# Optimization experiments

Hardware: AMD Instinct MI355X
Metric: run time of the kernel (lower is better)

The kernel has to match this reference:

```python
import jax, jax.numpy as jnp
import numpy as np
import itertools

N_OBJECTS = 8
NUM_VARS = 2  # num_total_variables


def _perm_indices(num_objects: int, num_vars: int):
    """Static permutation indices, matching AndLayer.build()."""
    perm_idxs = np.array(list(itertools.permutations(range(num_objects), num_vars)))  # [K, V]
    binary_idxs = np.stack(np.nonzero(1 - np.eye(num_vars))).T  # [V*(V-1), 2]
    binary_idxs = binary_idxs.reshape(num_vars, num_vars - 1, 2)
    perm_bidxs = perm_idxs[:, binary_idxs]  # [K, V, V-1, 2]
    shift = (perm_bidxs[..., 1] > perm_bidxs[..., 0]).astype(np.int64)
    perm_bidxs = np.stack([perm_bidxs[..., 0], perm_bidxs[..., 1] - shift], axis=-1)
    return perm_idxs, perm_bidxs


def setup_inputs() -> dict:
    key = jax.random.key(0)
    k0, k1, k2, k3 = jax.random.split(key, 4)
    B, N, P0, P1, P2, C = 32, N_OBJECTS, 64, 128, 64, 128
    V = NUM_VARS
    num_in = P0 + V * P1 + V * (V - 1) * P2  # 448
    return {
        "nullary_preds": jax.random.uniform(k0, (B, P0), dtype=jnp.float32),
        "unary_preds": jax.random.uniform(k1, (B, N, P1), dtype=jnp.float32),
        "binary_preds": jax.random.uniform(k2, (B, N, N - 1, P2), dtype=jnp.float32),
        "kernel": jax.random.normal(k3, (num_in, C), dtype=jnp.float32),
    }


def reference(nullary_preds, unary_preds, binary_preds, kernel):
    B = nullary_preds.shape[0]
    N = unary_preds.shape[1]
    perm_idxs, perm_bidxs = _perm_indices(N, NUM_VARS)
    K = perm_idxs.shape[0]  # number of permutations

    # [B, K, P0]
    perm_nullary = jnp.broadcast_to(nullary_preds[:, None], (B, K) + nullary_preds.shape[1:])
    # gather over object axis: [B, K, V, P1]
    perm_unary = unary_preds[:, perm_idxs]
    # gather (i, j') pairs: [B, K, V, V-1, P2]
    perm_binary = binary_preds[:, perm_bidxs[..., 0], perm_bidxs[..., 1]]

    in_tensor = jnp.concatenate(
        [perm_nullary,
         perm_unary.reshape(B, K, -1),
         perm_binary.reshape(B, K, -1)], axis=-1)  # [B, K, num_in]

    k = jnp.tanh(kernel)  # [num_in, C]
    # [B, K, num_in, C]
    weighted_truth = in_tensor[..., None] * k + (1.0 - jnp.square(k))
    conjuncts = jnp.max(jnp.min(weighted_truth, axis=2), axis=1)  # [B, C]
    return conjuncts
```

## Files before the change

### kernel.cpp

```cpp
#include <hip/hip_runtime.h>
#include <math.h>

#define BATCH   32
#define NOBJ    8
#define P0      64
#define P1      128
#define P2      64
#define COUT    128
#define KPERM   56
#define ITOT    448
#define NBGB    4
#define NIH     8
#define ISEG    (ITOT / NIH)
#define IC      8
#define NBLK    (KPERM * NBGB)
#define POISON  0xAAAAAAAAu

#define AMAX_ELEMS 4096
#define CNT_OFF    4096

__device__ __forceinline__ unsigned enc3(float f) {
    return __float_as_uint(f + 3.0f) | 0x80000000u;
}
__device__ __forceinline__ float dec3(unsigned u) {
    return __uint_as_float(u & 0x7FFFFFFFu) - 3.0f;
}
__device__ __forceinline__ float4 min4(float4 a, float4 b) {
    return make_float4(fminf(a.x, b.x), fminf(a.y, b.y),
                       fminf(a.z, b.z), fminf(a.w, b.w));
}
__device__ __forceinline__ float fast_tanh(float x) {
    const float e = __expf(2.0f * x);
    return fmaf(-2.0f, __builtin_amdgcn_rcpf(e + 1.0f), 1.0f);
}

__global__ __launch_bounds__(1024) void and_fused(const float* __restrict__ nullary,
                                                  const float* __restrict__ unary,
                                                  const float* __restrict__ binary,
                                                  const float* __restrict__ kern,
                                                  unsigned* __restrict__ ws,
                                                  float* __restrict__ out) {
    __shared__ float4 xs[ITOT][2];
    __shared__ float4 pm[NIH][COUT][2];
    __shared__ unsigned lastflag;

    unsigned* __restrict__ amax    = ws;
    unsigned* __restrict__ counter = ws + CNT_OFF;

    const int blk = blockIdx.x;
    const int k   = blk >> 2;
    const int bg  = blk & 3;
    const int tid = threadIdx.x;
    const int c   = tid & (COUT - 1);
    const int ih  = tid >> 7;

    const int a = k / (NOBJ - 1);
    const int r = k % (NOBJ - 1);
    const int bobj = r + (r >= a ? 1 : 0);
    const int m0 = bobj - (bobj > a ? 1 : 0);
    const int m1 = a - (a > bobj ? 1 : 0);

    float* xsf = (float*)xs;
    for (int e = tid; e < ITOT * 8; e += 1024) {
        const int i  = e >> 3;
        const int lb = e & 7;
        const int b  = bg * 8 + lb;
        float v;
        if (i < P0) {
            v = nullary[b * P0 + i];
        } else if (i < P0 + 2 * P1) {
            const int t2 = i - P0;
            const int vv = t2 >> 7;
            const int p  = t2 & (P1 - 1);
            const int n  = vv ? bobj : a;
            v = unary[(b * NOBJ + n) * P1 + p];
        } else {
            const int t2 = i - (P0 + 2 * P1);
            const int vv = t2 >> 6;
            const int p  = t2 & (P2 - 1);
            const int n  = vv ? bobj : a;
            const int m  = vv ? m1 : m0;
            v = binary[((b * NOBJ + n) * (NOBJ - 1) + m) * P2 + p];
        }
        xsf[e] = v;
    }
    __syncthreads();

    const float* __restrict__ kp = kern + c;
    float4 accL = make_float4(INFINITY, INFINITY, INFINITY, INFINITY);
    float4 accH = accL;

    const int ibase = ih * ISEG;
    #pragma unroll
    for (int i0 = ibase; i0 < ibase + ISEG; i0 += IC) {
        float kv[IC];
        #pragma unroll
        for (int u = 0; u < IC; ++u) kv[u] = kp[(i0 + u) << 7];
        #pragma unroll
        for (int u = 0; u < IC; ++u) {
            const float t  = fast_tanh(kv[u]);
            const float bs = fmaf(-t, t, 1.0f);
            const float4 xl = xs[i0 + u][0];
            const float4 xh = xs[i0 + u][1];
            accL.x = fminf(accL.x, fmaf(xl.x, t, bs));
            accL.y = fminf(accL.y, fmaf(xl.y, t, bs));
            accL.z = fminf(accL.z, fmaf(xl.z, t, bs));
            accL.w = fminf(accL.w, fmaf(xl.w, t, bs));
            accH.x = fminf(accH.x, fmaf(xh.x, t, bs));
            accH.y = fminf(accH.y, fmaf(xh.y, t, bs));
            accH.z = fminf(accH.z, fmaf(xh.z, t, bs));
            accH.w = fminf(accH.w, fmaf(xh.w, t, bs));
        }
    }

    pm[ih][c][0] = accL;
    pm[ih][c][1] = accH;
    __syncthreads();

    if (ih == 0) {
        float4 lo = pm[0][c][0], hi = pm[0][c][1];
        #pragma unroll
        for (int q = 1; q < NIH; ++q) {
            lo = min4(lo, pm[q][c][0]);
            hi = min4(hi, pm[q][c][1]);
        }
        unsigned* base = amax + (bg * 8) * COUT + c;
        atomicMax(base + 0 * COUT, enc3(lo.x));
        atomicMax(base + 1 * COUT, enc3(lo.y));
        atomicMax(base + 2 * COUT, enc3(lo.z));
        atomicMax(base + 3 * COUT, enc3(lo.w));
        atomicMax(base + 4 * COUT, enc3(hi.x));
        atomicMax(base + 5 * COUT, enc3(hi.y));
        atomicMax(base + 6 * COUT, enc3(hi.z));
        atomicMax(base + 7 * COUT, enc3(hi.w));
    }

    __syncthreads();
    if (tid == 0) {
        __threadfence();
        lastflag = (atomicAdd(counter, 1u) == POISON + (unsigned)(NBLK - 1));
    }
    __syncthreads();
    if (lastflag) {
        __threadfence();
        #pragma unroll
        for (int e = tid; e < AMAX_ELEMS; e += 1024) {
            const unsigned u = atomicAdd(amax + e, 0u);
            out[e] = dec3(u);
        }
    }
}

extern "C" void kernel_launch(void* const* d_in, const int* in_sizes, int n_in,
                              void* d_out, int out_size, void* d_ws, size_t ws_size,
                              hipStream_t stream) {
    const float* nullary = (const float*)d_in[0];
    const float* unary   = (const float*)d_in[1];
    const float* binary  = (const float*)d_in[2];
    const float* kern    = (const float*)d_in[3];
    float* out = (float*)d_out;

    and_fused<<<NBLK, 1024, 0, stream>>>(nullary, unary, binary, kern,
                                         (unsigned*)d_ws, out);
}
```

Measured before the change: 77.03 us.

## Split into gather/tanh prep kernel and main min-max kernel reading global staging

Splits the fused kernel into two launches. The first computes tanh(kernel) once into workspace and writes the gathered per-block input tiles to global memory. The second reads the precomputed tanh values and the 8-wide input vectors straight from global memory (no LDS staging), using paired min3 reductions with a smaller unroll. This drops the tanh that every block recomputed for each element and the shared-memory staging barrier. In exchange it adds a kernel launch and a global round-trip of about 3.2 MB for the gathered inputs.

New measurement: 77.33 us. About the same (+0.4%).

```diff
diff --git a/kernel.cpp b/kernel.cpp
--- a/kernel.cpp
+++ b/kernel.cpp
@@ -12,12 +12,15 @@
 #define NBGB    4
 #define NIH     8
 #define ISEG    (ITOT / NIH)
-#define IC      8
+#define IC      4
 #define NBLK    (KPERM * NBGB)
+#define XPB     (ITOT * 8)
 #define POISON  0xAAAAAAAAu
 
 #define AMAX_ELEMS 4096
 #define CNT_OFF    4096
+#define X_OFF      8192
+#define TK_OFF     (X_OFF + NBLK * XPB)
 
 __device__ __forceinline__ unsigned enc3(float f) {
     return __float_as_uint(f + 3.0f) | 0x80000000u;
@@ -25,43 +28,38 @@
 __device__ __forceinline__ float dec3(unsigned u) {
     return __uint_as_float(u & 0x7FFFFFFFu) - 3.0f;
 }
+__device__ __forceinline__ float min3f(float a, float b, float c) {
+    return fminf(fminf(a, b), c);
+}
 __device__ __forceinline__ float4 min4(float4 a, float4 b) {
     return make_float4(fminf(a.x, b.x), fminf(a.y, b.y),
                        fminf(a.z, b.z), fminf(a.w, b.w));
 }
-__device__ __forceinline__ float fast_tanh(float x) {
-    const float e = __expf(2.0f * x);
-    return fmaf(-2.0f, __builtin_amdgcn_rcpf(e + 1.0f), 1.0f);
-}
 
-__global__ __launch_bounds__(1024) void and_fused(const float* __restrict__ nullary,
-                                                  const float* __restrict__ unary,
-                                                  const float* __restrict__ binary,
-                                                  const float* __restrict__ kern,
-                                                  unsigned* __restrict__ ws,
-                                                  float* __restrict__ out) {
-    __shared__ float4 xs[ITOT][2];
-    __shared__ float4 pm[NIH][COUT][2];
-    __shared__ unsigned lastflag;
+typedef __attribute__((ext_vector_type(8))) float f32x8;
 
-    unsigned* __restrict__ amax    = ws;
-    unsigned* __restrict__ counter = ws + CNT_OFF;
+__global__ __launch_bounds__(1024) void prep_gather(const float* __restrict__ nullary,
+                                                    const float* __restrict__ unary,
+                                                    const float* __restrict__ binary,
+                                                    const float* __restrict__ kern,
+                                                    float* __restrict__ tk,
+                                                    float* __restrict__ X) {
+    const int blk = blockIdx.x;
+    const int tid = threadIdx.x;
 
-    const int blk = blockIdx.x;
-    const int k   = blk >> 2;
-    const int bg  = blk & 3;
-    const int tid = threadIdx.x;
-    const int c   = tid & (COUT - 1);
-    const int ih  = tid >> 7;
+    const int tkidx = blk * 1024 + tid;
+    if (tkidx < ITOT * COUT) tk[tkidx] = tanhf(kern[tkidx]);
 
+    const int k  = blk >> 2;
+    const int bg = blk & 3;
     const int a = k / (NOBJ - 1);
     const int r = k % (NOBJ - 1);
     const int bobj = r + (r >= a ? 1 : 0);
     const int m0 = bobj - (bobj > a ? 1 : 0);
     const int m1 = a - (a > bobj ? 1 : 0);
 
-    float* xsf = (float*)xs;
-    for (int e = tid; e < ITOT * 8; e += 1024) {
+    float* __restrict__ Xb = X + blk * XPB;
+    for (int e = tid; e < XPB; e += 1024) {
         const int i  = e >> 3;
         const int lb = e & 7;
         const int b  = bg * 8 + lb;
@@ -82,34 +80,57 @@
             const int m  = vv ? m1 : m0;
             v = binary[((b * NOBJ + n) * (NOBJ - 1) + m) * P2 + p];
         }
-        xsf[e] = v;
+        Xb[e] = v;
     }
-    __syncthreads();
+}
 
-    const float* __restrict__ kp = kern + c;
+__global__ __launch_bounds__(1024) void and_main(const float* __restrict__ tk,
+                                                 const float* __restrict__ X,
+                                                 unsigned* __restrict__ ws,
+                                                 float* __restrict__ out) {
+    __shared__ float4 pm[NIH][COUT][2];
+    __shared__ unsigned lastflag;
+
+    unsigned* __restrict__ amax    = ws;
+    unsigned* __restrict__ counter = ws + CNT_OFF;
+
+    const int blk = blockIdx.x;
+    const int bg  = blk & 3;
+    const int tid = threadIdx.x;
+    const int c   = tid & (COUT - 1);
+    const int ih  = tid >> 7;
+
+    const unsigned xoff =
+        (unsigned)__builtin_amdgcn_readfirstlane(blk * XPB + ih * ISEG * 8);
+    const f32x8* __restrict__ Xv = (const f32x8*)(X + xoff);
+
+    const float* __restrict__ tkp = tk + c;
+    const int ibase = ih * ISEG;
+
     float4 accL = make_float4(INFINITY, INFINITY, INFINITY, INFINITY);
     float4 accH = accL;
 
-    const int ibase = ih * ISEG;
-    #pragma unroll
-    for (int i0 = ibase; i0 < ibase + ISEG; i0 += IC) {
-        float kv[IC];
+    for (int c0 = 0; c0 < ISEG; c0 += IC) {
+        float  tv[IC];
+        f32x8  xv[IC];
         #pragma unroll
-        for (int u = 0; u < IC; ++u) kv[u] = kp[(i0 + u) << 7];
+        for (int u = 0; u < IC; ++u) tv[u] = tkp[(ibase + c0 + u) << 7];
         #pragma unroll
-        for (int u = 0; u < IC; ++u) {
-            const float t  = fast_tanh(kv[u]);
-            const float bs = fmaf(-t, t, 1.0f);
-            const float4 xl = xs[i0 + u][0];
-            const float4 xh = xs[i0 + u][1];
-            accL.x = fminf(accL.x, fmaf(xl.x, t, bs));
-            accL.y = fminf(accL.y, fmaf(xl.y, t, bs));
-            accL.z = fminf(accL.z, fmaf(xl.z, t, bs));
-            accL.w = fminf(accL.w, fmaf(xl.w, t, bs));
-            accH.x = fminf(accH.x, fmaf(xh.x, t, bs));
-            accH.y = fminf(accH.y, fmaf(xh.y, t, bs));
-            accH.z = fminf(accH.z, fmaf(xh.z, t, bs));
-            accH.w = fminf(accH.w, fmaf(xh.w, t, bs));
+        for (int u = 0; u < IC; ++u) xv[u] = Xv[c0 + u];
+        #pragma unroll
+        for (int u = 0; u < IC; u += 2) {
+            const float ta  = tv[u],   tb  = tv[u + 1];
+            const float bsa = fmaf(-ta, ta, 1.0f);
+            const float bsb = fmaf(-tb, tb, 1.0f);
+            const f32x8 xa = xv[u], xb = xv[u + 1];
+            accL.x = min3f(accL.x, fmaf(xa[0], ta, bsa), fmaf(xb[0], tb, bsb));
+            accL.y = min3f(accL.y, fmaf(xa[1], ta, bsa), fmaf(xb[1], tb, bsb));
+            accL.z = min3f(accL.z, fmaf(xa[2], ta, bsa), fmaf(xb[2], tb, bsb));
+            accL.w = min3f(accL.w, fmaf(xa[3], ta, bsa), fmaf(xb[3], tb, bsb));
+            accH.x = min3f(accH.x, fmaf(xa[4], ta, bsa), fmaf(xb[4], tb, bsb));
+            accH.y = min3f(accH.y, fmaf(xa[5], ta, bsa), fmaf(xb[5], tb, bsb));
+            accH.z = min3f(accH.z, fmaf(xa[6], ta, bsa), fmaf(xb[6], tb, bsb));
+            accH.w = min3f(accH.w, fmaf(xa[7], ta, bsa), fmaf(xb[7], tb, bsb));
         }
     }
 
@@ -160,6 +181,10 @@
     const float* kern    = (const float*)d_in[3];
     float* out = (float*)d_out;
 
-    and_fused<<<NBLK, 1024, 0, stream>>>(nullary, unary, binary, kern,
-                                         (unsigned*)d_ws, out);
+    unsigned* ws = (unsigned*)d_ws;
+    float* X  = (float*)d_ws + X_OFF;
+    float* tk = (float*)d_ws + TK_OFF;
+
+    prep_gather<<<NBLK, 1024, 0, stream>>>(nullary, unary, binary, kern, tk, X);
+    and_main<<<NBLK, 1024, 0, stream>>>(tk, X, ws, out);
 }
```
